# Kernel tuning notes

Measured on AMD Instinct MI355X. Metric: run time of the kernel, lower is better.

Reference implementation:

```python
import jax, jax.numpy as jnp
import numpy as np

D, LEN_IN, LEN_OUT = 2, 1, 10
H1, H2 = 32, 32
B, T = 4096, 512
F_IN = D * LEN_IN          # 2
F_OUT = D * LEN_OUT        # 20


def setup_inputs() -> dict:
    key = jax.random.key(0)
    ks = jax.random.split(key, 12)
    s = 1.0 / np.sqrt(H1)  # PyTorch default init scale for LSTMCell/Linear
    u = lambda k, shape: jax.random.uniform(k, shape, jnp.float32, -s, s)
    return {
        "x": jax.random.normal(ks[0], (B, T, F_IN), jnp.float32),
        # LSTMCell 1 (input 2 -> hidden 32); gate order i,f,g,o stacked on dim 0
        "W_ih1": u(ks[1], (4 * H1, F_IN)),
        "W_hh1": u(ks[2], (4 * H1, H1)),
        "b_ih1": u(ks[3], (4 * H1,)),
        "b_hh1": u(ks[4], (4 * H1,)),
        # LSTMCell 2 (32 -> 32)
        "W_ih2": u(ks[5], (4 * H2, H1)),
        "W_hh2": u(ks[6], (4 * H2, H2)),
        "b_ih2": u(ks[7], (4 * H2,)),
        "b_hh2": u(ks[8], (4 * H2,)),
        # Final linear 32 -> 20
        "W_out": u(ks[9], (F_OUT, H2)),
        "b_out": u(ks[10], (F_OUT,)),
    }


def _lstm_cell(x, h, c, W_ih, W_hh, b):
    # gates: [B, 4H]; PyTorch gate order i, f, g, o
    gates = x @ W_ih.T + h @ W_hh.T + b
    i, f, g, o = jnp.split(gates, 4, axis=-1)
    i, f, o = jax.nn.sigmoid(i), jax.nn.sigmoid(f), jax.nn.sigmoid(o)
    g = jnp.tanh(g)
    c_new = f * c + i * g
    h_new = o * jnp.tanh(c_new)
    return h_new, c_new


def reference(x, W_ih1, W_hh1, b_ih1, b_hh1, W_ih2, W_hh2, b_ih2, b_hh2, W_out, b_out):
    b1 = b_ih1 + b_hh1
    b2 = b_ih2 + b_hh2
    Bsz = x.shape[0]
    h1 = jnp.zeros((Bsz, H1), x.dtype)
    c1 = jnp.zeros((Bsz, H1), x.dtype)
    h2 = jnp.zeros((Bsz, H2), x.dtype)
    c2 = jnp.zeros((Bsz, H2), x.dtype)

    def step(carry, x_t):
        h1, c1, h2, c2 = carry
        h1, c1 = _lstm_cell(x_t, h1, c1, W_ih1, W_hh1, b1)
        h2, c2 = _lstm_cell(h1, h2, c2, W_ih2, W_hh2, b2)
        out_t = h2 @ W_out.T + b_out  # [B, 20]
        return (h1, c1, h2, c2), out_t

    xs = jnp.swapaxes(x, 0, 1)  # [T, B, F_IN]
    _, outs = jax.lax.scan(step, (h1, c1, h2, c2), xs)  # outs: [T, B, 20]
    outs = jnp.swapaxes(outs, 0, 1)  # [B, T, 20]
    return outs.reshape(Bsz, x.shape[1], D, LEN_OUT)
```

## Files before the change

### kernel.cpp

```cpp
#include <hip/hip_runtime.h>
#include <hip/hip_fp16.h>

#define TLEN 512
#define HDIM 32
#define FOUT 20
#define HST  40

typedef __attribute__((ext_vector_type(8))) short bf16x8;
typedef __attribute__((ext_vector_type(4))) float f32x4;
typedef __attribute__((ext_vector_type(4))) short s16x4;

__device__ __forceinline__ float sigm(float v) {
  float e = __builtin_amdgcn_exp2f(-1.4426950408889634f * v);
  return __builtin_amdgcn_rcpf(1.0f + e);
}
__device__ __forceinline__ float tanh_f(float v) {
  float e = __builtin_amdgcn_exp2f(2.8853900817779268f * v);
  return 1.0f - 2.0f * __builtin_amdgcn_rcpf(1.0f + e);
}
__device__ __forceinline__ void hilo(float v, short& h, short& l) {
  unsigned u = __builtin_bit_cast(unsigned, v);
  unsigned r = u + 0x7fffu + ((u >> 16) & 1u);
  h = (short)(r >> 16);
  float hf = __builtin_bit_cast(float, r & 0xffff0000u);
  float res = v - hf;
  unsigned u2 = __builtin_bit_cast(unsigned, res);
  unsigned r2 = u2 + 0x7fffu + ((u2 >> 16) & 1u);
  l = (short)(r2 >> 16);
}

__device__ __forceinline__ void barrier_lgkm() {
  asm volatile("s_waitcnt lgkmcnt(0)\n\ts_barrier" ::: "memory");
}

__device__ __forceinline__ bf16x8 read_h(const short* buf, int off) {
  return *(const bf16x8*)(buf + off);
}

__device__ __forceinline__ float lstm_update(const f32x4& g, float& c) {
  float iv = sigm(g[0]), fv = sigm(g[1]), gv = tanh_f(g[2]), ov = sigm(g[3]);
  c = fv * c + iv * gv;
  return ov * tanh_f(c);
}

__global__ __launch_bounds__(1024, 1) void lstm_seq_kernel(
    const float* __restrict__ xg,
    const float* __restrict__ Wih1, const float* __restrict__ Whh1,
    const float* __restrict__ bih1, const float* __restrict__ bhh1,
    const float* __restrict__ Wih2, const float* __restrict__ Whh2,
    const float* __restrict__ bih2, const float* __restrict__ bhh2,
    const float* __restrict__ Wout, const float* __restrict__ bout,
    float* __restrict__ out)
{
  __shared__ __half xl[16 * 1028];
  __shared__ short h1hiB[2][16 * HST], h1loB[2][16 * HST];
  __shared__ short h2hiB[2][16 * HST], h2loB[2][16 * HST];

  const int tid  = threadIdx.x;
  const int w    = tid >> 6;
  const int lane = tid & 63;
  const int n    = lane & 15;
  const int q    = lane >> 4;
  const int q4   = q * 4;
  const int q8   = q * 8;
  const int b0   = blockIdx.x * 16;
  const bool isL1 = (w < 8);
  const int wr   = w & 7;
  const int p    = w & 1;
  const int pr   = (w >> 1) & 3;

  for (int idx = tid; idx < 16 * 1024; idx += 1024) {
    int row = idx >> 10, col = idx & 1023;
    xl[row * 1028 + col] = __float2half(xg[((size_t)(b0 + row) << 10) + col]);
  }

  const int og = (n & 3) * HDIM + 4 * wr + (n >> 2);
  bf16x8 WAh, WAl, WBh, WBl;
  float bc[4], wx0[4], wx1[4];
  f32x4 bcv = {0.f, 0.f, 0.f, 0.f};
  f32x4 bocv = {0.f, 0.f, 0.f, 0.f};
  const f32x4 zv4 = {0.f, 0.f, 0.f, 0.f};
  bf16x8 WoH = {0,0,0,0,0,0,0,0}, WoL = {0,0,0,0,0,0,0,0};
  if (isL1) {
    #pragma unroll
    for (int j = 0; j < 8; j++) {
      short hh, ll;
      hilo(Whh1[og * HDIM + q8 + j], hh, ll); WAh[j] = hh; WAl[j] = ll;
    }
    #pragma unroll
    for (int r = 0; r < 4; r++) {
      int gr = r * HDIM + 4 * wr + q;
      bc[r]  = bih1[gr] + bhh1[gr];
      wx0[r] = Wih1[gr * 2 + 0];
      wx1[r] = Wih1[gr * 2 + 1];
    }
  } else {
    #pragma unroll
    for (int j = 0; j < 8; j++) {
      short hh, ll;
      hilo(Wih2[og * HDIM + q8 + j], hh, ll); WAh[j] = hh; WAl[j] = ll;
      hilo(Whh2[og * HDIM + q8 + j], hh, ll); WBh[j] = hh; WBl[j] = ll;
    }
    #pragma unroll
    for (int r = 0; r < 4; r++) {
      int gr = r * HDIM + 4 * wr + q;
      bcv[r] = bih2[gr] + bhh2[gr];
      int orow = 16 * p + q4 + r;
      bocv[r] = (orow < FOUT) ? bout[orow] : 0.0f;
    }
    int orow = 16 * p + n;
    if (orow < FOUT) {
      #pragma unroll
      for (int j = 0; j < 8; j++) {
        short hh, ll;
        hilo(Wout[orow * HDIM + q8 + j], hh, ll); WoH[j] = hh; WoL[j] = ll;
      }
    }
  }

  const int hoff = n * HST + 4 * wr + q;
  const int aoff = n * HST + q8;
  float c = 0.0f;

  bf16x8 h1h = {0,0,0,0,0,0,0,0}, h1l = {0,0,0,0,0,0,0,0};
  bf16x8 h2h = {0,0,0,0,0,0,0,0}, h2l = {0,0,0,0,0,0,0,0};

  __syncthreads();

  if (isL1) {
    __half2 hv = *(const __half2*)&xl[n * 1028];
    float xv0 = __half2float(hv.x), xv1 = __half2float(hv.y);
    f32x4 g1;
    #pragma unroll
    for (int r = 0; r < 4; r++) g1[r] = fmaf(xv1, wx1[r], fmaf(xv0, wx0[r], bc[r]));
    float h1n = lstm_update(g1, c);
    short hh, ll; hilo(h1n, hh, ll);
    h1hiB[0][hoff] = hh; h1loB[0][hoff] = ll;
  }
  barrier_lgkm();
  h1h = read_h(h1hiB[0], aoff);
  h1l = read_h(h1loB[0], aoff);

#define STEP(T, PAR, DS3, XV0, XV1)                                              \
  {                                                                               \
    if (isL1) {                                                                   \
      f32x4 g1;                                                                   \
      _Pragma("unroll") for (int r = 0; r < 4; r++)                               \
        g1[r] = fmaf((XV1), wx1[r], fmaf((XV0), wx0[r], bc[r]));                  \
      g1 = __builtin_amdgcn_mfma_f32_16x16x32_bf16(WAh, h1h, g1, 0, 0, 0);        \
      g1 = __builtin_amdgcn_mfma_f32_16x16x32_bf16(WAl, h1h, g1, 0, 0, 0);        \
      g1 = __builtin_amdgcn_mfma_f32_16x16x32_bf16(WAh, h1l, g1, 0, 0, 0);        \
      float h1n = lstm_update(g1, c);                                             \
      short hh, ll; hilo(h1n, hh, ll);                                            \
      h1hiB[PAR][hoff] = hh; h1loB[PAR][hoff] = ll;                               \
    } else {                                                                      \
      f32x4 ga = __builtin_amdgcn_mfma_f32_16x16x32_bf16(WAh, h1h, bcv, 0, 0, 0); \
      f32x4 gb = __builtin_amdgcn_mfma_f32_16x16x32_bf16(WBh, h2h, zv4, 0, 0, 0); \
      ga = __builtin_amdgcn_mfma_f32_16x16x32_bf16(WAl, h1h, ga, 0, 0, 0);        \
      gb = __builtin_amdgcn_mfma_f32_16x16x32_bf16(WBl, h2h, gb, 0, 0, 0);        \
      ga = __builtin_amdgcn_mfma_f32_16x16x32_bf16(WAh, h1l, ga, 0, 0, 0);        \
      gb = __builtin_amdgcn_mfma_f32_16x16x32_bf16(WBh, h2l, gb, 0, 0, 0);        \
      f32x4 g2;                                                                   \
      _Pragma("unroll") for (int r = 0; r < 4; r++) g2[r] = ga[r] + gb[r];        \
      float h2n = lstm_update(g2, c);                                             \
      short hh, ll; hilo(h2n, hh, ll);                                            \
      h2hiB[PAR][hoff] = hh; h2loB[PAR][hoff] = ll;                               \
    }                                                                             \
    barrier_lgkm();                                   \
    if (isL1) {                                                                   \
      h1h = read_h(h1hiB[PAR], aoff);                                             \
      h1l = read_h(h1loB[PAR], aoff);                                             \
    } else {                                                                      \
             \
      if ((DS3) >= 0 && pr == (DS3)) {                                            \
        f32x4 ao = __builtin_amdgcn_mfma_f32_16x16x32_bf16(WoH, h2h, bocv, 0, 0, 0);\
        ao = __builtin_amdgcn_mfma_f32_16x16x32_bf16(WoL, h2h, ao, 0, 0, 0);      \
        ao = __builtin_amdgcn_mfma_f32_16x16x32_bf16(WoH, h2l, ao, 0, 0, 0);      \
        if (p == 0 || q == 0) {                                                   \
          float4 st = { ao[0], ao[1], ao[2], ao[3] };                             \
          *(float4*)&out[((size_t)(b0 + n) * TLEN + ((T) - 2)) * FOUT + 16 * p + q4] = st; \
        }                                                                         \
      }                                                                           \
      h1h = read_h(h1hiB[PAR], aoff);                                             \
      h1l = read_h(h1loB[PAR], aoff);                                             \
      h2h = read_h(h2hiB[PAR], aoff);                                             \
      h2l = read_h(h2loB[PAR], aoff);                                             \
    }                                                                             \
  }

  {
    float a0 = 0.f, a1 = 0.f;
    if (isL1) { __half2 hv = *(const __half2*)&xl[n * 1028 + 2]; a0 = __half2float(hv.x); a1 = __half2float(hv.y); }
    STEP(1, 1, -1, a0, a1);
    if (isL1) { __half2 hv = *(const __half2*)&xl[n * 1028 + 4]; a0 = __half2float(hv.x); a1 = __half2float(hv.y); }
    STEP(2, 0, 0, a0, a1);
    if (isL1) { __half2 hv = *(const __half2*)&xl[n * 1028 + 6]; a0 = __half2float(hv.x); a1 = __half2float(hv.y); }
    STEP(3, 1, 1, a0, a1);
  }

  float xv[8] = {0.f, 0.f, 0.f, 0.f, 0.f, 0.f, 0.f, 0.f};
  for (int t = 4; t < TLEN; t += 4) {
    if (isL1) {
      const short* xp = (const short*)xl + n * 1028 + 2 * t;
      s16x4 xa = *(const s16x4*)xp;
      s16x4 xb = *(const s16x4*)(xp + 4);
      #pragma unroll
      for (int j = 0; j < 4; j++) {
        xv[j]     = __half2float(__builtin_bit_cast(__half, (short)xa[j]));
        xv[4 + j] = __half2float(__builtin_bit_cast(__half, (short)xb[j]));
      }
    }
    STEP(t + 0, 0, 2, xv[0], xv[1]);
    STEP(t + 1, 1, 3, xv[2], xv[3]);
    STEP(t + 2, 0, 0, xv[4], xv[5]);
    STEP(t + 3, 1, 1, xv[6], xv[7]);
  }
#undef STEP

  if (!isL1) {
    f32x4 ga = __builtin_amdgcn_mfma_f32_16x16x32_bf16(WAh, h1h, bcv, 0, 0, 0);
    f32x4 gb = __builtin_amdgcn_mfma_f32_16x16x32_bf16(WBh, h2h, zv4, 0, 0, 0);
    ga = __builtin_amdgcn_mfma_f32_16x16x32_bf16(WAl, h1h, ga, 0, 0, 0);
    gb = __builtin_amdgcn_mfma_f32_16x16x32_bf16(WBl, h2h, gb, 0, 0, 0);
    ga = __builtin_amdgcn_mfma_f32_16x16x32_bf16(WAh, h1l, ga, 0, 0, 0);
    gb = __builtin_amdgcn_mfma_f32_16x16x32_bf16(WBh, h2l, gb, 0, 0, 0);
    f32x4 g2;
    #pragma unroll
    for (int r = 0; r < 4; r++) g2[r] = ga[r] + gb[r];
    float h2n = lstm_update(g2, c);
    short hh, ll; hilo(h2n, hh, ll);
    h2hiB[0][hoff] = hh; h2loB[0][hoff] = ll;
  }
  barrier_lgkm();
  if (!isL1) {
    if (pr == 2) {
      const int s = TLEN - 2;
      f32x4 ao = __builtin_amdgcn_mfma_f32_16x16x32_bf16(WoH, h2h, bocv, 0, 0, 0);
      ao = __builtin_amdgcn_mfma_f32_16x16x32_bf16(WoL, h2h, ao, 0, 0, 0);
      ao = __builtin_amdgcn_mfma_f32_16x16x32_bf16(WoH, h2l, ao, 0, 0, 0);
      if (p == 0 || q == 0) {
        float4 st = { ao[0], ao[1], ao[2], ao[3] };
        *(float4*)&out[((size_t)(b0 + n) * TLEN + s) * FOUT + 16 * p + q4] = st;
      }
    }
    if (pr == 3) {
      h2h = read_h(h2hiB[0], aoff);
      h2l = read_h(h2loB[0], aoff);
      const int s = TLEN - 1;
      f32x4 ao = __builtin_amdgcn_mfma_f32_16x16x32_bf16(WoH, h2h, bocv, 0, 0, 0);
      ao = __builtin_amdgcn_mfma_f32_16x16x32_bf16(WoL, h2h, ao, 0, 0, 0);
      ao = __builtin_amdgcn_mfma_f32_16x16x32_bf16(WoH, h2l, ao, 0, 0, 0);
      if (p == 0 || q == 0) {
        float4 st = { ao[0], ao[1], ao[2], ao[3] };
        *(float4*)&out[((size_t)(b0 + n) * TLEN + s) * FOUT + 16 * p + q4] = st;
      }
    }
  }
}

extern "C" void kernel_launch(void* const* d_in, const int* in_sizes, int n_in,
                              void* d_out, int out_size, void* d_ws, size_t ws_size,
                              hipStream_t stream) {
  const float* xg   = (const float*)d_in[0];
  const float* Wih1 = (const float*)d_in[1];
  const float* Whh1 = (const float*)d_in[2];
  const float* bih1 = (const float*)d_in[3];
  const float* bhh1 = (const float*)d_in[4];
  const float* Wih2 = (const float*)d_in[5];
  const float* Whh2 = (const float*)d_in[6];
  const float* bih2 = (const float*)d_in[7];
  const float* bhh2 = (const float*)d_in[8];
  const float* Wout = (const float*)d_in[9];
  const float* bout = (const float*)d_in[10];
  float* out = (float*)d_out;

  hipLaunchKernelGGL(lstm_seq_kernel, dim3(256), dim3(1024), 0, stream,
                     xg, Wih1, Whh1, bih1, bhh1, Wih2, Whh2, bih2, bhh2, Wout, bout, out);
}
```

Baseline: 436.7 us.

## Halve batch per block to 8 rows, doubling blocks and gate tiles per wave

Each block now handles 8 batch rows with 512 threads (8 waves) instead of 16 rows with 1024 threads. The grid becomes 512 blocks, so all CUs can be filled on the 256-CU part and several blocks can share a CU. Each wave now computes two gate tiles and selects its result per lane by the upper half of n. Half the MFMA columns are redundant, duplicating rows 0-7, so each wave does twice the MFMA work per step. In exchange, more independent recurrences run concurrently, hiding the serial latency of each step.

New measurement: 536.4 us. 1.23x slower.

```diff
diff --git a/kernel.cpp b/kernel.cpp
--- a/kernel.cpp
+++ b/kernel.cpp
@@ -43,7 +43,7 @@
   return ov * tanh_f(c);
 }
 
-__global__ __launch_bounds__(1024, 1) void lstm_seq_kernel(
+__global__ __launch_bounds__(512, 4) void lstm_seq_kernel(
     const float* __restrict__ xg,
     const float* __restrict__ Wih1, const float* __restrict__ Whh1,
     const float* __restrict__ bih1, const float* __restrict__ bhh1,
@@ -52,9 +52,9 @@
     const float* __restrict__ Wout, const float* __restrict__ bout,
     float* __restrict__ out)
 {
-  __shared__ __half xl[16 * 1028];
-  __shared__ short h1hiB[2][16 * HST], h1loB[2][16 * HST];
-  __shared__ short h2hiB[2][16 * HST], h2loB[2][16 * HST];
+  __shared__ __half xl[8 * 1028];
+  __shared__ short h1hiB[2][8 * HST], h1loB[2][8 * HST];
+  __shared__ short h2hiB[2][8 * HST], h2loB[2][8 * HST];
 
   const int tid  = threadIdx.x;
   const int w    = tid >> 6;
@@ -63,48 +63,57 @@
   const int q    = lane >> 4;
   const int q4   = q * 4;
   const int q8   = q * 8;
-  const int b0   = blockIdx.x * 16;
-  const bool isL1 = (w < 8);
-  const int wr   = w & 7;
+  const int b0   = blockIdx.x * 8;
+  const bool isL1 = (w < 4);
+  const int wr   = w & 3;
+  const int ub   = wr * 8;
   const int p    = w & 1;
-  const int pr   = (w >> 1) & 3;
-
-  for (int idx = tid; idx < 16 * 1024; idx += 1024) {
+  const int pr   = (w >> 1) & 1;
+  const bool hiHalf = (n & 8) != 0;
+
+  for (int idx = tid; idx < 8 * 1024; idx += 512) {
     int row = idx >> 10, col = idx & 1023;
     xl[row * 1028 + col] = __float2half(xg[((size_t)(b0 + row) << 10) + col]);
   }
 
-  const int og = (n & 3) * HDIM + 4 * wr + (n >> 2);
-  bf16x8 WAh, WAl, WBh, WBl;
-  float bc[4], wx0[4], wx1[4];
-  f32x4 bcv = {0.f, 0.f, 0.f, 0.f};
-  f32x4 bocv = {0.f, 0.f, 0.f, 0.f};
-  const f32x4 zv4 = {0.f, 0.f, 0.f, 0.f};
+  const int og0 = (n & 3) * HDIM + ub + (n >> 2);
+  const int og1 = og0 + 4;
+  bf16x8 WA0h, WA0l, WA1h, WA1l;
+  bf16x8 WB0h = {0,0,0,0,0,0,0,0}, WB0l = {0,0,0,0,0,0,0,0};
+  bf16x8 WB1h = {0,0,0,0,0,0,0,0}, WB1l = {0,0,0,0,0,0,0,0};
+  float bc0[4], bc1[4], wx00[4], wx10[4], wx01[4], wx11[4];
+  f32x4 bcv0 = {0.f,0.f,0.f,0.f}, bcv1 = {0.f,0.f,0.f,0.f};
+  f32x4 bocv = {0.f,0.f,0.f,0.f};
+  const f32x4 zv4 = {0.f,0.f,0.f,0.f};
   bf16x8 WoH = {0,0,0,0,0,0,0,0}, WoL = {0,0,0,0,0,0,0,0};
   if (isL1) {
     #pragma unroll
     for (int j = 0; j < 8; j++) {
       short hh, ll;
-      hilo(Whh1[og * HDIM + q8 + j], hh, ll); WAh[j] = hh; WAl[j] = ll;
+      hilo(Whh1[og0 * HDIM + q8 + j], hh, ll); WA0h[j] = hh; WA0l[j] = ll;
+      hilo(Whh1[og1 * HDIM + q8 + j], hh, ll); WA1h[j] = hh; WA1l[j] = ll;
     }
     #pragma unroll
     for (int r = 0; r < 4; r++) {
-      int gr = r * HDIM + 4 * wr + q;
-      bc[r]  = bih1[gr] + bhh1[gr];
-      wx0[r] = Wih1[gr * 2 + 0];
-      wx1[r] = Wih1[gr * 2 + 1];
+      int gr0 = r * HDIM + ub + q, gr1 = gr0 + 4;
+      bc0[r]  = bih1[gr0] + bhh1[gr0];  bc1[r]  = bih1[gr1] + bhh1[gr1];
+      wx00[r] = Wih1[gr0 * 2 + 0];      wx01[r] = Wih1[gr1 * 2 + 0];
+      wx10[r] = Wih1[gr0 * 2 + 1];      wx11[r] = Wih1[gr1 * 2 + 1];
     }
   } else {
     #pragma unroll
     for (int j = 0; j < 8; j++) {
       short hh, ll;
-      hilo(Wih2[og * HDIM + q8 + j], hh, ll); WAh[j] = hh; WAl[j] = ll;
-      hilo(Whh2[og * HDIM + q8 + j], hh, ll); WBh[j] = hh; WBl[j] = ll;
+      hilo(Wih2[og0 * HDIM + q8 + j], hh, ll); WA0h[j] = hh; WA0l[j] = ll;
+      hilo(Wih2[og1 * HDIM + q8 + j], hh, ll); WA1h[j] = hh; WA1l[j] = ll;
+      hilo(Whh2[og0 * HDIM + q8 + j], hh, ll); WB0h[j] = hh; WB0l[j] = ll;
+      hilo(Whh2[og1 * HDIM + q8 + j], hh, ll); WB1h[j] = hh; WB1l[j] = ll;
     }
     #pragma unroll
     for (int r = 0; r < 4; r++) {
-      int gr = r * HDIM + 4 * wr + q;
-      bcv[r] = bih2[gr] + bhh2[gr];
+      int gr0 = r * HDIM + ub + q, gr1 = gr0 + 4;
+      bcv0[r] = bih2[gr0] + bhh2[gr0];
+      bcv1[r] = bih2[gr1] + bhh2[gr1];
       int orow = 16 * p + q4 + r;
       bocv[r] = (orow < FOUT) ? bout[orow] : 0.0f;
     }
@@ -118,8 +127,8 @@
     }
   }
 
-  const int hoff = n * HST + 4 * wr + q;
-  const int aoff = n * HST + q8;
+  const int hoff = (n & 7) * HST + ub + (hiHalf ? 4 : 0) + q;
+  const int aoff = (n & 7) * HST + q8;
   float c = 0.0f;
 
   bf16x8 h1h = {0,0,0,0,0,0,0,0}, h1l = {0,0,0,0,0,0,0,0};
@@ -128,11 +137,16 @@
   __syncthreads();
 
   if (isL1) {
-    __half2 hv = *(const __half2*)&xl[n * 1028];
+    __half2 hv = *(const __half2*)&xl[(n & 7) * 1028];
     float xv0 = __half2float(hv.x), xv1 = __half2float(hv.y);
     f32x4 g1;
     #pragma unroll
-    for (int r = 0; r < 4; r++) g1[r] = fmaf(xv1, wx1[r], fmaf(xv0, wx0[r], bc[r]));
+    for (int r = 0; r < 4; r++) {
+      float b  = hiHalf ? bc1[r]  : bc0[r];
+      float w0 = hiHalf ? wx01[r] : wx00[r];
+      float w1 = hiHalf ? wx11[r] : wx10[r];
+      g1[r] = fmaf(xv1, w1, fmaf(xv0, w0, b));
+    }
     float h1n = lstm_update(g1, c);
     short hh, ll; hilo(h1n, hh, ll);
     h1hiB[0][hoff] = hh; h1loB[0][hoff] = ll;
@@ -141,28 +155,46 @@
   h1h = read_h(h1hiB[0], aoff);
   h1l = read_h(h1loB[0], aoff);
 
-#define STEP(T, PAR, DS3, XV0, XV1)                                              \
+#define STEP(T, PAR, DS1, XV0, XV1)                                               \
   {                                                                               \
     if (isL1) {                                                                   \
-      f32x4 g1;                                                                   \
+      f32x4 g1t0, g1t1;                                                           \
+      _Pragma("unroll") for (int r = 0; r < 4; r++) {                             \
+        g1t0[r] = fmaf((XV1), wx10[r], fmaf((XV0), wx00[r], bc0[r]));             \
+        g1t1[r] = fmaf((XV1), wx11[r], fmaf((XV0), wx01[r], bc1[r]));             \
+      }                                                                           \
+      g1t0 = __builtin_amdgcn_mfma_f32_16x16x32_bf16(WA0h, h1h, g1t0, 0, 0, 0);   \
+      g1t1 = __builtin_amdgcn_mfma_f32_16x16x32_bf16(WA1h, h1h, g1t1, 0, 0, 0);   \
+      g1t0 = __builtin_amdgcn_mfma_f32_16x16x32_bf16(WA0l, h1h, g1t0, 0, 0, 0);   \
+      g1t1 = __builtin_amdgcn_mfma_f32_16x16x32_bf16(WA1l, h1h, g1t1, 0, 0, 0);   \
+      g1t0 = __builtin_amdgcn_mfma_f32_16x16x32_bf16(WA0h, h1l, g1t0, 0, 0, 0);   \
+      g1t1 = __builtin_amdgcn_mfma_f32_16x16x32_bf16(WA1h, h1l, g1t1, 0, 0, 0);   \
+      f32x4 g;                                                                    \
       _Pragma("unroll") for (int r = 0; r < 4; r++)                               \
-        g1[r] = fmaf((XV1), wx1[r], fmaf((XV0), wx0[r], bc[r]));                  \
-      g1 = __builtin_amdgcn_mfma_f32_16x16x32_bf16(WAh, h1h, g1, 0, 0, 0);        \
-      g1 = __builtin_amdgcn_mfma_f32_16x16x32_bf16(WAl, h1h, g1, 0, 0, 0);        \
-      g1 = __builtin_amdgcn_mfma_f32_16x16x32_bf16(WAh, h1l, g1, 0, 0, 0);        \
-      float h1n = lstm_update(g1, c);                                             \
+        g[r] = hiHalf ? g1t1[r] : g1t0[r];                                        \
+      float h1n = lstm_update(g, c);                                              \
       short hh, ll; hilo(h1n, hh, ll);                                            \
       h1hiB[PAR][hoff] = hh; h1loB[PAR][hoff] = ll;                               \
     } else {                                                                      \
-      f32x4 ga = __builtin_amdgcn_mfma_f32_16x16x32_bf16(WAh, h1h, bcv, 0, 0, 0); \
-      f32x4 gb = __builtin_amdgcn_mfma_f32_16x16x32_bf16(WBh, h2h, zv4, 0, 0, 0); \
-      ga = __builtin_amdgcn_mfma_f32_16x16x32_bf16(WAl, h1h, ga, 0, 0, 0);        \
-      gb = __builtin_amdgcn_mfma_f32_16x16x32_bf16(WBl, h2h, gb, 0, 0, 0);        \
-      ga = __builtin_amdgcn_mfma_f32_16x16x32_bf16(WAh, h1l, ga, 0, 0, 0);        \
-      gb = __builtin_amdgcn_mfma_f32_16x16x32_bf16(WBh, h2l, gb, 0, 0, 0);        \
-      f32x4 g2;                                                                   \
-      _Pragma("unroll") for (int r = 0; r < 4; r++) g2[r] = ga[r] + gb[r];        \
-      float h2n = lstm_update(g2, c);                                             \
+      f32x4 ga0 = __builtin_amdgcn_mfma_f32_16x16x32_bf16(WA0h, h1h, bcv0, 0, 0, 0); \
+      f32x4 gb0 = __builtin_amdgcn_mfma_f32_16x16x32_bf16(WB0h, h2h, zv4, 0, 0, 0);  \
+      f32x4 ga1 = __builtin_amdgcn_mfma_f32_16x16x32_bf16(WA1h, h1h, bcv1, 0, 0, 0); \
+      f32x4 gb1 = __builtin_amdgcn_mfma_f32_16x16x32_bf16(WB1h, h2h, zv4, 0, 0, 0);  \
+      ga0 = __builtin_amdgcn_mfma_f32_16x16x32_bf16(WA0l, h1h, ga0, 0, 0, 0);     \
+      gb0 = __builtin_amdgcn_mfma_f32_16x16x32_bf16(WB0l, h2h, gb0, 0, 0, 0);     \
+      ga1 = __builtin_amdgcn_mfma_f32_16x16x32_bf16(WA1l, h1h, ga1, 0, 0, 0);     \
+      gb1 = __builtin_amdgcn_mfma_f32_16x16x32_bf16(WB1l, h2h, gb1, 0, 0, 0);     \
+      ga0 = __builtin_amdgcn_mfma_f32_16x16x32_bf16(WA0h, h1l, ga0, 0, 0, 0);     \
+      gb0 = __builtin_amdgcn_mfma_f32_16x16x32_bf16(WB0h, h2l, gb0, 0, 0, 0);     \
+      ga1 = __builtin_amdgcn_mfma_f32_16x16x32_bf16(WA1h, h1l, ga1, 0, 0, 0);     \
+      gb1 = __builtin_amdgcn_mfma_f32_16x16x32_bf16(WB1h, h2l, gb1, 0, 0, 0);     \
+      f32x4 g;                                                                    \
+      _Pragma("unroll") for (int r = 0; r < 4; r++) {                             \
+        float t0 = ga0[r] + gb0[r];                                               \
+        float t1 = ga1[r] + gb1[r];                                               \
+        g[r] = hiHalf ? t1 : t0;                                                  \
+      }                                                                           \
+      float h2n = lstm_update(g, c);                                              \
       short hh, ll; hilo(h2n, hh, ll);                                            \
       h2hiB[PAR][hoff] = hh; h2loB[PAR][hoff] = ll;                               \
     }                                                                             \
@@ -171,12 +203,11 @@
       h1h = read_h(h1hiB[PAR], aoff);                                             \
       h1l = read_h(h1loB[PAR], aoff);                                             \
     } else {                                                                      \
-             \
-      if ((DS3) >= 0 && pr == (DS3)) {                                            \
-        f32x4 ao = __builtin_amdgcn_mfma_f32_16x16x32_bf16(WoH, h2h, bocv, 0, 0, 0);\
+      if ((DS1) >= 0 && pr == (DS1)) {                                            \
+        f32x4 ao = __builtin_amdgcn_mfma_f32_16x16x32_bf16(WoH, h2h, bocv, 0, 0, 0); \
         ao = __builtin_amdgcn_mfma_f32_16x16x32_bf16(WoL, h2h, ao, 0, 0, 0);      \
         ao = __builtin_amdgcn_mfma_f32_16x16x32_bf16(WoH, h2l, ao, 0, 0, 0);      \
-        if (p == 0 || q == 0) {                                                   \
+        if ((p == 0 || q == 0) && n < 8) {                                        \
           float4 st = { ao[0], ao[1], ao[2], ao[3] };                             \
           *(float4*)&out[((size_t)(b0 + n) * TLEN + ((T) - 2)) * FOUT + 16 * p + q4] = st; \
         }                                                                         \
@@ -190,18 +221,18 @@
 
   {
     float a0 = 0.f, a1 = 0.f;
-    if (isL1) { __half2 hv = *(const __half2*)&xl[n * 1028 + 2]; a0 = __half2float(hv.x); a1 = __half2float(hv.y); }
+    if (isL1) { __half2 hv = *(const __half2*)&xl[(n & 7) * 1028 + 2]; a0 = __half2float(hv.x); a1 = __half2float(hv.y); }
     STEP(1, 1, -1, a0, a1);
-    if (isL1) { __half2 hv = *(const __half2*)&xl[n * 1028 + 4]; a0 = __half2float(hv.x); a1 = __half2float(hv.y); }
+    if (isL1) { __half2 hv = *(const __half2*)&xl[(n & 7) * 1028 + 4]; a0 = __half2float(hv.x); a1 = __half2float(hv.y); }
     STEP(2, 0, 0, a0, a1);
-    if (isL1) { __half2 hv = *(const __half2*)&xl[n * 1028 + 6]; a0 = __half2float(hv.x); a1 = __half2float(hv.y); }
+    if (isL1) { __half2 hv = *(const __half2*)&xl[(n & 7) * 1028 + 6]; a0 = __half2float(hv.x); a1 = __half2float(hv.y); }
     STEP(3, 1, 1, a0, a1);
   }
 
   float xv[8] = {0.f, 0.f, 0.f, 0.f, 0.f, 0.f, 0.f, 0.f};
   for (int t = 4; t < TLEN; t += 4) {
     if (isL1) {
-      const short* xp = (const short*)xl + n * 1028 + 2 * t;
+      const short* xp = (const short*)xl + (n & 7) * 1028 + 2 * t;
       s16x4 xa = *(const s16x4*)xp;
       s16x4 xb = *(const s16x4*)(xp + 4);
       #pragma unroll
@@ -210,47 +241,57 @@
         xv[4 + j] = __half2float(__builtin_bit_cast(__half, (short)xb[j]));
       }
     }
-    STEP(t + 0, 0, 2, xv[0], xv[1]);
-    STEP(t + 1, 1, 3, xv[2], xv[3]);
+    STEP(t + 0, 0, 0, xv[0], xv[1]);
+    STEP(t + 1, 1, 1, xv[2], xv[3]);
     STEP(t + 2, 0, 0, xv[4], xv[5]);
     STEP(t + 3, 1, 1, xv[6], xv[7]);
   }
 #undef STEP
 
   if (!isL1) {
-    f32x4 ga = __builtin_amdgcn_mfma_f32_16x16x32_bf16(WAh, h1h, bcv, 0, 0, 0);
-    f32x4 gb = __builtin_amdgcn_mfma_f32_16x16x32_bf16(WBh, h2h, zv4, 0, 0, 0);
-    ga = __builtin_amdgcn_mfma_f32_16x16x32_bf16(WAl, h1h, ga, 0, 0, 0);
-    gb = __builtin_amdgcn_mfma_f32_16x16x32_bf16(WBl, h2h, gb, 0, 0, 0);
-    ga = __builtin_amdgcn_mfma_f32_16x16x32_bf16(WAh, h1l, ga, 0, 0, 0);
-    gb = __builtin_amdgcn_mfma_f32_16x16x32_bf16(WBh, h2l, gb, 0, 0, 0);
-    f32x4 g2;
-    #pragma unroll
-    for (int r = 0; r < 4; r++) g2[r] = ga[r] + gb[r];
-    float h2n = lstm_update(g2, c);
+    f32x4 ga0 = __builtin_amdgcn_mfma_f32_16x16x32_bf16(WA0h, h1h, bcv0, 0, 0, 0);
+    f32x4 gb0 = __builtin_amdgcn_mfma_f32_16x16x32_bf16(WB0h, h2h, zv4, 0, 0, 0);
+    f32x4 ga1 = __builtin_amdgcn_mfma_f32_16x16x32_bf16(WA1h, h1h, bcv1, 0, 0, 0);
+    f32x4 gb1 = __builtin_amdgcn_mfma_f32_16x16x32_bf16(WB1h, h2h, zv4, 0, 0, 0);
+    ga0 = __builtin_amdgcn_mfma_f32_16x16x32_bf16(WA0l, h1h, ga0, 0, 0, 0);
+    gb0 = __builtin_amdgcn_mfma_f32_16x16x32_bf16(WB0l, h2h, gb0, 0, 0, 0);
+    ga1 = __builtin_amdgcn_mfma_f32_16x16x32_bf16(WA1l, h1h, ga1, 0, 0, 0);
+    gb1 = __builtin_amdgcn_mfma_f32_16x16x32_bf16(WB1l, h2h, gb1, 0, 0, 0);
+    ga0 = __builtin_amdgcn_mfma_f32_16x16x32_bf16(WA0h, h1l, ga0, 0, 0, 0);
+    gb0 = __builtin_amdgcn_mfma_f32_16x16x32_bf16(WB0h, h2l, gb0, 0, 0, 0);
+    ga1 = __builtin_amdgcn_mfma_f32_16x16x32_bf16(WA1h, h1l, ga1, 0, 0, 0);
+    gb1 = __builtin_amdgcn_mfma_f32_16x16x32_bf16(WB1h, h2l, gb1, 0, 0, 0);
+    f32x4 g;
+    #pragma unroll
+    for (int r = 0; r < 4; r++) {
+      float t0 = ga0[r] + gb0[r];
+      float t1 = ga1[r] + gb1[r];
+      g[r] = hiHalf ? t1 : t0;
+    }
+    float h2n = lstm_update(g, c);
     short hh, ll; hilo(h2n, hh, ll);
     h2hiB[0][hoff] = hh; h2loB[0][hoff] = ll;
   }
   barrier_lgkm();
   if (!isL1) {
-    if (pr == 2) {
+    if (pr == 0) {
       const int s = TLEN - 2;
       f32x4 ao = __builtin_amdgcn_mfma_f32_16x16x32_bf16(WoH, h2h, bocv, 0, 0, 0);
       ao = __builtin_amdgcn_mfma_f32_16x16x32_bf16(WoL, h2h, ao, 0, 0, 0);
       ao = __builtin_amdgcn_mfma_f32_16x16x32_bf16(WoH, h2l, ao, 0, 0, 0);
-      if (p == 0 || q == 0) {
+      if ((p == 0 || q == 0) && n < 8) {
         float4 st = { ao[0], ao[1], ao[2], ao[3] };
         *(float4*)&out[((size_t)(b0 + n) * TLEN + s) * FOUT + 16 * p + q4] = st;
       }
     }
-    if (pr == 3) {
+    if (pr == 1) {
       h2h = read_h(h2hiB[0], aoff);
       h2l = read_h(h2loB[0], aoff);
       const int s = TLEN - 1;
       f32x4 ao = __builtin_amdgcn_mfma_f32_16x16x32_bf16(WoH, h2h, bocv, 0, 0, 0);
       ao = __builtin_amdgcn_mfma_f32_16x16x32_bf16(WoL, h2h, ao, 0, 0, 0);
       ao = __builtin_amdgcn_mfma_f32_16x16x32_bf16(WoH, h2l, ao, 0, 0, 0);
-      if (p == 0 || q == 0) {
+      if ((p == 0 || q == 0) && n < 8) {
         float4 st = { ao[0], ao[1], ao[2], ao[3] };
         *(float4*)&out[((size_t)(b0 + n) * TLEN + s) * FOUT + 16 * p + q4] = st;
       }
@@ -274,6 +315,6 @@
   const float* bout = (const float*)d_in[10];
   float* out = (float*)d_out;
 
-  hipLaunchKernelGGL(lstm_seq_kernel, dim3(256), dim3(1024), 0, stream,
+  hipLaunchKernelGGL(lstm_seq_kernel, dim3(512), dim3(512), 0, stream,
                      xg, Wih1, Whh1, bih1, bhh1, Wih2, Whh2, bih2, bhh2, Wout, bout, out);
 }
```
